# Kernel tuning notes

Measured on AMD Instinct MI355X. Metric: run time of the kernel, lower is better.

The kernel has to match this reference:

```python
import jax, jax.numpy as jnp
import numpy as np

EMBED_DIM = 1024
NUM_HEADS = 16
HEAD_DIM = EMBED_DIM // NUM_HEADS


def setup_inputs() -> dict:
    key = jax.random.key(0)
    ks = jax.random.split(key, 9)
    B, S, D = 4, 2048, EMBED_DIM
    scale = 1.0 / np.sqrt(D)
    inp = {
        "x": jax.random.normal(ks[0], (B, S, D), dtype=jnp.float32),
        "wq": jax.random.normal(ks[1], (D, D), dtype=jnp.float32) * scale,
        "bq": jnp.zeros((D,), dtype=jnp.float32),
        "wk": jax.random.normal(ks[2], (D, D), dtype=jnp.float32) * scale,
        "bk": jnp.zeros((D,), dtype=jnp.float32),
        "wv": jax.random.normal(ks[3], (D, D), dtype=jnp.float32) * scale,
        "bv": jnp.zeros((D,), dtype=jnp.float32),
        "wo": jax.random.normal(ks[4], (D, D), dtype=jnp.float32) * scale,
        "bo": jnp.zeros((D,), dtype=jnp.float32),
    }
    return inp


def reference(x, wq, bq, wk, bk, wv, bv, wo, bo):
    B, S, D = x.shape
    H, Hd = NUM_HEADS, HEAD_DIM

    def split_heads(t):
        # [B, S, D] -> [B, H, S, Hd]
        return t.reshape(B, S, H, Hd).transpose(0, 2, 1, 3)

    q = split_heads(x @ wq.T + bq)
    k = split_heads(x @ wk.T + bk)
    v = split_heads(x @ wv.T + bv)

    scores = jnp.einsum("bhqd,bhkd->bhqk", q, k) / jnp.sqrt(jnp.float32(Hd))
    attn = jax.nn.softmax(scores, axis=-1)
    out = jnp.einsum("bhqk,bhkd->bhqd", attn, v)  # [B, H, S, Hd]
    out = out.transpose(0, 2, 1, 3).reshape(B, S, D)
    return out @ wo.T + bo
```

## Files before the change

kernel.cpp:

```cpp
#include <hip/hip_runtime.h>
#include <hip/hip_bf16.h>
#include <hip/hip_fp16.h>

typedef _Float16 f16;
typedef f16 f16x8 __attribute__((ext_vector_type(8)));
typedef f16 f16x4 __attribute__((ext_vector_type(4)));
typedef f16 f16x2 __attribute__((ext_vector_type(2)));
typedef float f32x4 __attribute__((ext_vector_type(4)));
typedef float f32x16 __attribute__((ext_vector_type(16)));
typedef unsigned int u32x4 __attribute__((ext_vector_type(4)));
typedef unsigned int u32x2 __attribute__((ext_vector_type(2)));

#define MFMA16(a, b, c) __builtin_amdgcn_mfma_f32_16x16x32_f16(a, b, c, 0, 0, 0)
#define MFMA32(a, b, c) __builtin_amdgcn_mfma_f32_32x32x16_f16(a, b, c, 0, 0, 0)

constexpr int BB = 4, SS = 2048, DD = 1024, HH = 16, HDIM = 64;
constexpr int MM = BB * SS;
constexpr float QSCALE = 0.125f * 1.44269504088896340736f;


__device__ __forceinline__ void gl_lds16(const void* g, void* l) {
  __builtin_amdgcn_global_load_lds((const __attribute__((address_space(1))) void*)g,
                                   (__attribute__((address_space(3))) void*)l, 16, 0, 0);
}

__global__ __launch_bounds__(256) void cvt_all_kernel(const float* __restrict__ x,
                                                      const float* __restrict__ w0,
                                                      const float* __restrict__ w1,
                                                      const float* __restrict__ w2,
                                                      const float* __restrict__ w3,
                                                      f16* xh, f16* o0, f16* o1,
                                                      f16* o2, f16* o3) {
  int bid = blockIdx.x;
  const float* in; f16* out; int idx;
  if (bid < MM * DD / 4 / 256) {
    in = x; out = xh; idx = bid * 256 + threadIdx.x;
  } else {
    int wb = bid - MM * DD / 4 / 256;
    int which = wb >> 10;
    in = which == 0 ? w0 : which == 1 ? w1 : which == 2 ? w2 : w3;
    out = which == 0 ? o0 : which == 1 ? o1 : which == 2 ? o2 : o3;
    idx = (wb & 1023) * 256 + threadIdx.x;
  }
  f32x4 v = reinterpret_cast<const f32x4*>(in)[idx];
  f16x4 o;
  o[0] = (f16)v[0]; o[1] = (f16)v[1]; o[2] = (f16)v[2]; o[3] = (f16)v[3];
  reinterpret_cast<f16x4*>(out)[idx] = o;
}

__device__ __forceinline__ int swz(int row, int slot) {
  return row * 64 + ((slot ^ (row & 7)) << 3);
}

__global__ __launch_bounds__(256) void qkv_kernel(const f16* __restrict__ A,
                                                  const f16* __restrict__ Wq,
                                                  const f16* __restrict__ Wk,
                                                  const f16* __restrict__ Wv,
                                                  const float* __restrict__ bq,
                                                  const float* __restrict__ bk,
                                                  const float* __restrict__ bv,
                                                  f16* __restrict__ Qo,
                                                  f16* __restrict__ Ko,
                                                  f16* __restrict__ Vo) {
  constexpr int K = 1024;
  __shared__ __align__(16) char smem_raw[128 * 136 * 2];
  f16* As = (f16*)smem_raw;
  f16* Ws = As + 128 * 64;

  const int mat = blockIdx.x >> 3;
  const f16* W = mat == 0 ? Wq : (mat == 1 ? Wk : Wv);
  const float* bias = mat == 0 ? bq : (mat == 1 ? bk : bv);
  const float scale = mat == 0 ? QSCALE : 1.0f;

  const int tid = threadIdx.x;
  const int m0 = blockIdx.y * 128, n0 = (blockIdx.x & 7) * 128;
  const int w = tid >> 6, lane = tid & 63;
  const int wm = (w >> 1) * 64, wn = (w & 1) * 64;
  const int g = lane >> 4, r = lane & 15;
  const int srow = lane >> 3;
  const int sslot = (lane & 7) ^ srow;

  f32x4 acc[4][4] = {};

  for (int k0 = 0; k0 < K; k0 += 64) {
#pragma unroll
    for (int i = 0; i < 4; ++i) {
      int rbase = w * 32 + i * 8;
      gl_lds16(A + (size_t)(m0 + rbase + srow) * K + k0 + sslot * 8, As + rbase * 64);
      gl_lds16(W + (size_t)(n0 + rbase + srow) * K + k0 + sslot * 8, Ws + rbase * 64);
    }
    __syncthreads();

#pragma unroll
    for (int ks = 0; ks < 2; ++ks) {
      f16x8 af[4], bf[4];
#pragma unroll
      for (int i = 0; i < 4; ++i) {
        af[i] = *reinterpret_cast<const f16x8*>(As + swz(wm + i * 16 + r, (ks << 2) | g));
        bf[i] = *reinterpret_cast<const f16x8*>(Ws + swz(wn + i * 16 + r, (ks << 2) | g));
      }
#pragma unroll
      for (int i = 0; i < 4; ++i)
#pragma unroll
        for (int j = 0; j < 4; ++j)
          acc[i][j] = MFMA16(af[i], bf[j], acc[i][j]);
    }
    __syncthreads();
  }

  if (mat == 0) {
#pragma unroll
    for (int i = 0; i < 4; ++i)
#pragma unroll
      for (int j = 0; j < 4; ++j)
#pragma unroll
        for (int q = 0; q < 4; ++q) {
          int gm = m0 + wm + i * 16 + g * 4 + q;
          int gn = n0 + wn + j * 16 + r;
          float v = (acc[i][j][q] + bias[gn]) * scale;
          int b = gm >> 11, s = gm & 2047;
          int h = gn >> 6, hd = gn & 63;
          Qo[(((size_t)(b * HH + h)) * SS + s) * HDIM + hd] = (f16)v;
        }
  } else if (mat == 1) {
#pragma unroll
    for (int i = 0; i < 4; ++i)
#pragma unroll
      for (int j = 0; j < 4; ++j)
#pragma unroll
        for (int q = 0; q < 4; ++q) {
          int gm = m0 + wm + i * 16 + g * 4 + q;
          int gn = n0 + wn + j * 16 + r;
          float v = acc[i][j][q] + bias[gn];
          int b = gm >> 11, s = gm & 2047;
          int h = gn >> 6, hd = gn & 63;
          int tile = s >> 6, row = s & 63, slot = hd >> 3, w8 = hd & 7;
          size_t off = ((((size_t)(b * HH + h) * 32 + tile) * 8 + slot) * 64 + row) * 8 + w8;
          Ko[off] = (f16)v;
        }
  } else {
    __syncthreads();
    f16* T = (f16*)smem_raw;
#pragma unroll
    for (int i = 0; i < 4; ++i)
#pragma unroll
      for (int j = 0; j < 4; ++j)
#pragma unroll
        for (int q = 0; q < 4; ++q) {
          int ml = wm + i * 16 + g * 4 + q;
          int nl = wn + j * 16 + r;
          T[nl * 136 + ml] = (f16)(acc[i][j][q] + bias[n0 + nl]);
        }
    __syncthreads();
    const int b = m0 >> 11, sbase = m0 & 2047;
#pragma unroll
    for (int it = 0; it < 8; ++it) {
      int cid = it * 256 + tid;
      int hd_l = cid & 127, sl = (cid >> 7) & 7, tl = cid >> 10;
      u32x4 v = *reinterpret_cast<const u32x4*>(T + hd_l * 136 + tl * 64 + sl * 8);
      int gn = n0 + hd_l, h = gn >> 6, hd = gn & 63;
      int tile = (sbase >> 6) + tl;
      size_t off = ((((size_t)(b * HH + h) * 32 + tile) * 8 + sl) * 64 + hd) * 8;
      *reinterpret_cast<u32x4*>(Vo + off) = v;
    }
  }
}

__global__ __launch_bounds__(256) void oproj_kernel(const f16* __restrict__ A,
                                                    const f16* __restrict__ W,
                                                    const float* __restrict__ bias,
                                                    float* __restrict__ Out) {
  constexpr int K = 1024, N = 1024;
  __shared__ __align__(16) f16 As[128 * 64];
  __shared__ __align__(16) f16 Ws[128 * 64];

  const int tid = threadIdx.x;
  const int m0 = blockIdx.y * 128, n0 = blockIdx.x * 128;
  const int w = tid >> 6, lane = tid & 63;
  const int wm = (w >> 1) * 64, wn = (w & 1) * 64;
  const int g = lane >> 4, r = lane & 15;
  const int srow = lane >> 3;
  const int sslot = (lane & 7) ^ srow;

  f32x4 acc[4][4] = {};

  for (int k0 = 0; k0 < K; k0 += 64) {
#pragma unroll
    for (int i = 0; i < 4; ++i) {
      int rbase = w * 32 + i * 8;
      gl_lds16(A + (size_t)(m0 + rbase + srow) * K + k0 + sslot * 8, As + rbase * 64);
      gl_lds16(W + (size_t)(n0 + rbase + srow) * K + k0 + sslot * 8, Ws + rbase * 64);
    }
    __syncthreads();

#pragma unroll
    for (int ks = 0; ks < 2; ++ks) {
      f16x8 af[4], bf[4];
#pragma unroll
      for (int i = 0; i < 4; ++i) {
        af[i] = *reinterpret_cast<const f16x8*>(As + swz(wm + i * 16 + r, (ks << 2) | g));
        bf[i] = *reinterpret_cast<const f16x8*>(Ws + swz(wn + i * 16 + r, (ks << 2) | g));
      }
#pragma unroll
      for (int i = 0; i < 4; ++i)
#pragma unroll
        for (int j = 0; j < 4; ++j)
          acc[i][j] = MFMA16(af[i], bf[j], acc[i][j]);
    }
    __syncthreads();
  }

#pragma unroll
  for (int i = 0; i < 4; ++i)
#pragma unroll
    for (int j = 0; j < 4; ++j)
#pragma unroll
      for (int q = 0; q < 4; ++q) {
        int gm = m0 + wm + i * 16 + g * 4 + q;
        int gn = n0 + wn + j * 16 + r;
        Out[(size_t)gm * N + gn] = acc[i][j][q] + bias[gn];
      }
}

__global__ __launch_bounds__(256, 4) void attn_kernel(const f16* __restrict__ Q,
                                                      const f16* __restrict__ K,
                                                      const f16* __restrict__ Vt,
                                                      f16* __restrict__ AO) {
  __shared__ __align__(16) f16 Kls[2][8 * 512];
  __shared__ __align__(16) f16 Vls[2][8 * 512];
  __shared__ __align__(16) float Lw[4][32];

  const int tid = threadIdx.x;
  const int w = tid >> 6, lane = tid & 63;
  const int q31 = lane & 31;
  const int h = lane >> 5;
  const int bh = blockIdx.y;
  const int q0 = blockIdx.x * 128;

  const f16* Kg = K + (size_t)bh * (SS * HDIM);
  const f16* Vg = Vt + (size_t)bh * (SS * HDIM);
  const int s0 = 2 * w;
  const int rofs = h * 512 + q31 * 8;

  const f16* Qg = Q + ((size_t)bh * SS + q0 + w * 32 + q31) * HDIM + 8 * h;
  f16x8 qf[4];
#pragma unroll
  for (int m = 0; m < 4; ++m)
    qf[m] = *reinterpret_cast<const f16x8*>(Qg + 16 * m);

  f32x16 oacc[2] = {};
  float lsum = 0.f;

#pragma unroll
  for (int i = 0; i < 2; ++i) {
    int s_idx = s0 + i;
    gl_lds16(Kg + (size_t)(s_idx * 64 + lane) * 8, &Kls[0][s_idx * 512]);
    gl_lds16(Vg + (size_t)(s_idx * 64 + lane) * 8, &Vls[0][s_idx * 512]);
  }
  __syncthreads();

  for (int t = 0; t < SS / 64; ++t) {
    const int cur = t & 1;
    if (t < SS / 64 - 1) {
#pragma unroll
      for (int i = 0; i < 2; ++i) {
        int s_idx = s0 + i;
        gl_lds16(Kg + (size_t)((t + 1) * 512 + s_idx * 64 + lane) * 8,
                 &Kls[cur ^ 1][s_idx * 512]);
        gl_lds16(Vg + (size_t)((t + 1) * 512 + s_idx * 64 + lane) * 8,
                 &Vls[cur ^ 1][s_idx * 512]);
      }
    }
    const f16* Kc = &Kls[cur][0];
    const f16* Vc = &Vls[cur][0];

#pragma unroll
    for (int kb = 0; kb < 2; ++kb) {
      f32x16 sacc = {};
      __builtin_amdgcn_s_setprio(1);
#pragma unroll
      for (int m = 0; m < 4; ++m) {
        f16x8 kf = *reinterpret_cast<const f16x8*>(Kc + m * 1024 + kb * 256 + rofs);
        sacc = MFMA32(kf, qf[m], sacc);
      }
      __builtin_amdgcn_s_setprio(0);

      unsigned pk[8];
#pragma unroll
      for (int rp = 0; rp < 4; ++rp)
#pragma unroll
        for (int p = 0; p < 2; ++p) {
          float e0 = __builtin_amdgcn_exp2f(sacc[4 * rp + 2 * p]);
          float e1 = __builtin_amdgcn_exp2f(sacc[4 * rp + 2 * p + 1]);
          pk[2 * rp + p] = __builtin_bit_cast(unsigned, __builtin_amdgcn_cvt_pkrtz(e0, e1));
        }

      f16x2 s01 = __builtin_bit_cast(f16x2, pk[0]) + __builtin_bit_cast(f16x2, pk[1]);
      f16x2 s23 = __builtin_bit_cast(f16x2, pk[2]) + __builtin_bit_cast(f16x2, pk[3]);
      f16x2 s45 = __builtin_bit_cast(f16x2, pk[4]) + __builtin_bit_cast(f16x2, pk[5]);
      f16x2 s67 = __builtin_bit_cast(f16x2, pk[6]) + __builtin_bit_cast(f16x2, pk[7]);
      f16x2 st = (s01 + s23) + (s45 + s67);
      lsum += (float)st[0] + (float)st[1];

#pragma unroll
      for (int jl = 0; jl < 2; ++jl) {
        auto sw0 = __builtin_amdgcn_permlane32_swap(pk[4 * jl + 0], pk[4 * jl + 2], false, false);
        auto sw1 = __builtin_amdgcn_permlane32_swap(pk[4 * jl + 1], pk[4 * jl + 3], false, false);
        u32x4 fw = {(unsigned)sw0[0], (unsigned)sw1[0], (unsigned)sw0[1], (unsigned)sw1[1]};
        f16x8 pa = __builtin_bit_cast(f16x8, fw);
        const int j = 2 * kb + jl;
        __builtin_amdgcn_s_setprio(1);
#pragma unroll
        for (int vb = 0; vb < 2; ++vb) {
          f16x8 vbf = *reinterpret_cast<const f16x8*>(Vc + j * 1024 + vb * 256 + rofs);
          oacc[vb] = MFMA32(pa, vbf, oacc[vb]);
        }
        __builtin_amdgcn_s_setprio(0);
      }
    }
    __syncthreads();
  }

  lsum += __shfl_xor(lsum, 32, 64);
  if (h == 0) Lw[w][q31] = 1.0f / lsum;

  f32x4 li[4];
#pragma unroll
  for (int rq = 0; rq < 4; ++rq)
    li[rq] = *reinterpret_cast<const f32x4*>(&Lw[w][8 * rq + 4 * h]);

  const int b = bh >> 4, head = bh & 15;
  f16* aobase = AO + ((size_t)(b * SS + q0 + 32 * w)) * DD + head * 64 + q31;
#pragma unroll
  for (int vb = 0; vb < 2; ++vb)
#pragma unroll
    for (int reg = 0; reg < 16; ++reg) {
      int q = (reg & 3) + 8 * (reg >> 2) + 4 * h;
      aobase[(size_t)q * DD + 32 * vb] = (f16)(oacc[vb][reg] * li[reg >> 2][reg & 3]);
    }
}

extern "C" void kernel_launch(void* const* d_in, const int* in_sizes, int n_in,
                              void* d_out, int out_size, void* d_ws, size_t ws_size,
                              hipStream_t stream) {
  (void)in_sizes; (void)n_in; (void)out_size; (void)ws_size;
  const float* x  = (const float*)d_in[0];
  const float* wq = (const float*)d_in[1];
  const float* bq = (const float*)d_in[2];
  const float* wk = (const float*)d_in[3];
  const float* bk = (const float*)d_in[4];
  const float* wv = (const float*)d_in[5];
  const float* bv = (const float*)d_in[6];
  const float* wo = (const float*)d_in[7];
  const float* bo = (const float*)d_in[8];
  float* out = (float*)d_out;

  char* ws = (char*)d_ws;
  f16* xh  = (f16*)ws; ws += (size_t)MM * DD * 2;
  f16* wqh = (f16*)ws; ws += (size_t)DD * DD * 2;
  f16* wkh = (f16*)ws; ws += (size_t)DD * DD * 2;
  f16* wvh = (f16*)ws; ws += (size_t)DD * DD * 2;
  f16* woh = (f16*)ws; ws += (size_t)DD * DD * 2;
  f16* Qb  = (f16*)ws; ws += (size_t)MM * DD * 2;
  f16* Kb  = (f16*)ws; ws += (size_t)MM * DD * 2;
  f16* Vtb = (f16*)ws; ws += (size_t)MM * DD * 2;
  f16* AOb = (f16*)ws; ws += (size_t)MM * DD * 2;

  cvt_all_kernel<<<MM * DD / 4 / 256 + 4 * (DD * DD / 4 / 256), 256, 0, stream>>>(
      x, wq, wk, wv, wo, xh, wqh, wkh, wvh, woh);

  qkv_kernel<<<dim3(24, MM / 128), 256, 0, stream>>>(xh, wqh, wkh, wvh, bq, bk, bv, Qb, Kb, Vtb);

  attn_kernel<<<dim3(SS / 128, BB * HH), 256, 0, stream>>>(Qb, Kb, Vtb, AOb);

  oproj_kernel<<<dim3(DD / 128, MM / 128), 256, 0, stream>>>(AOb, woh, bo, out);
}
```

Baseline: 197.1 us.

## Stream K/V from global into registers, remap block order, coalesce K stores

The attention kernel drops its LDS double buffer and barriers and loads K and V fragments straight from global into registers, prefetching the next 32-key tile while the current one computes. All three GEMM and attention kernels switch to 1D grids with a remapped block order, so that consecutive blocks share the same rows or heads for better L2 locality. The K projection epilogue now goes through an LDS transpose and writes 16-byte vectors instead of scalars, and the LDS tile pitch grows to 152. Per-wave global loads give up the data sharing that LDS provided across the four waves, and they rely on the cache to absorb the repeated traffic.

```diff
diff --git a/kernel.cpp b/kernel.cpp
--- a/kernel.cpp
+++ b/kernel.cpp
@@ -63,17 +63,22 @@
                                                   f16* __restrict__ Ko,
                                                   f16* __restrict__ Vo) {
   constexpr int K = 1024;
-  __shared__ __align__(16) char smem_raw[128 * 136 * 2];
+  constexpr int TS = 152;
+  __shared__ __align__(16) char smem_raw[128 * TS * 2];
   f16* As = (f16*)smem_raw;
   f16* Ws = As + 128 * 64;
 
-  const int mat = blockIdx.x >> 3;
+  const int p = blockIdx.x;
+  const int bx = (p >> 3) % 24;
+  const int by = (p & 7) + 8 * ((p >> 3) / 24);
+
+  const int mat = bx >> 3;
   const f16* W = mat == 0 ? Wq : (mat == 1 ? Wk : Wv);
   const float* bias = mat == 0 ? bq : (mat == 1 ? bk : bv);
   const float scale = mat == 0 ? QSCALE : 1.0f;
 
   const int tid = threadIdx.x;
-  const int m0 = blockIdx.y * 128, n0 = (blockIdx.x & 7) * 128;
+  const int m0 = by * 128, n0 = (bx & 7) * 128;
   const int w = tid >> 6, lane = tid & 63;
   const int wm = (w >> 1) * 64, wn = (w & 1) * 64;
   const int g = lane >> 4, r = lane & 15;
@@ -123,22 +128,6 @@
           Qo[(((size_t)(b * HH + h)) * SS + s) * HDIM + hd] = (f16)v;
         }
   } else if (mat == 1) {
-#pragma unroll
-    for (int i = 0; i < 4; ++i)
-#pragma unroll
-      for (int j = 0; j < 4; ++j)
-#pragma unroll
-        for (int q = 0; q < 4; ++q) {
-          int gm = m0 + wm + i * 16 + g * 4 + q;
-          int gn = n0 + wn + j * 16 + r;
-          float v = acc[i][j][q] + bias[gn];
-          int b = gm >> 11, s = gm & 2047;
-          int h = gn >> 6, hd = gn & 63;
-          int tile = s >> 6, row = s & 63, slot = hd >> 3, w8 = hd & 7;
-          size_t off = ((((size_t)(b * HH + h) * 32 + tile) * 8 + slot) * 64 + row) * 8 + w8;
-          Ko[off] = (f16)v;
-        }
-  } else {
     __syncthreads();
     f16* T = (f16*)smem_raw;
 #pragma unroll
@@ -149,7 +138,33 @@
         for (int q = 0; q < 4; ++q) {
           int ml = wm + i * 16 + g * 4 + q;
           int nl = wn + j * 16 + r;
-          T[nl * 136 + ml] = (f16)(acc[i][j][q] + bias[n0 + nl]);
+          T[ml * TS + nl] = (f16)(acc[i][j][q] + bias[n0 + nl]);
+        }
+    __syncthreads();
+    const int b = m0 >> 11, sbase = m0 & 2047;
+#pragma unroll
+    for (int it = 0; it < 8; ++it) {
+      int cid = it * 256 + tid;
+      int row_s = cid & 127, ns = cid >> 7;
+      u32x4 v = *reinterpret_cast<const u32x4*>(T + row_s * TS + ns * 8);
+      int gn0 = n0 + ns * 8;
+      int h = gn0 >> 6, slot = (gn0 & 63) >> 3;
+      int tile = (sbase >> 6) + (row_s >> 6), row = row_s & 63;
+      size_t off = ((((size_t)(b * HH + h) * 32 + tile) * 8 + slot) * 64 + row) * 8;
+      *reinterpret_cast<u32x4*>(Ko + off) = v;
+    }
+  } else {
+    __syncthreads();
+    f16* T = (f16*)smem_raw;
+#pragma unroll
+    for (int i = 0; i < 4; ++i)
+#pragma unroll
+      for (int j = 0; j < 4; ++j)
+#pragma unroll
+        for (int q = 0; q < 4; ++q) {
+          int ml = wm + i * 16 + g * 4 + q;
+          int nl = wn + j * 16 + r;
+          T[nl * TS + ml] = (f16)(acc[i][j][q] + bias[n0 + nl]);
         }
     __syncthreads();
     const int b = m0 >> 11, sbase = m0 & 2047;
@@ -157,7 +172,7 @@
     for (int it = 0; it < 8; ++it) {
       int cid = it * 256 + tid;
       int hd_l = cid & 127, sl = (cid >> 7) & 7, tl = cid >> 10;
-      u32x4 v = *reinterpret_cast<const u32x4*>(T + hd_l * 136 + tl * 64 + sl * 8);
+      u32x4 v = *reinterpret_cast<const u32x4*>(T + hd_l * TS + tl * 64 + sl * 8);
       int gn = n0 + hd_l, h = gn >> 6, hd = gn & 63;
       int tile = (sbase >> 6) + tl;
       size_t off = ((((size_t)(b * HH + h) * 32 + tile) * 8 + sl) * 64 + hd) * 8;
@@ -174,8 +189,12 @@
   __shared__ __align__(16) f16 As[128 * 64];
   __shared__ __align__(16) f16 Ws[128 * 64];
 
+  const int p = blockIdx.x;
+  const int bx = (p >> 3) & 7;
+  const int by = (p & 7) | ((p >> 6) << 3);
+
   const int tid = threadIdx.x;
-  const int m0 = blockIdx.y * 128, n0 = blockIdx.x * 128;
+  const int m0 = by * 128, n0 = bx * 128;
   const int w = tid >> 6, lane = tid & 63;
   const int wm = (w >> 1) * 64, wn = (w & 1) * 64;
   const int g = lane >> 4, r = lane & 15;
@@ -226,21 +245,20 @@
                                                       const f16* __restrict__ K,
                                                       const f16* __restrict__ Vt,
                                                       f16* __restrict__ AO) {
-  __shared__ __align__(16) f16 Kls[2][8 * 512];
-  __shared__ __align__(16) f16 Vls[2][8 * 512];
-  __shared__ __align__(16) float Lw[4][32];
+  __shared__ float Lw[4][32];
+
+  const int p = blockIdx.x;
+  const int qx = (p >> 3) & 15;
+  const int bh = (p & 7) | ((p >> 7) << 3);
+  const int q0 = qx * 128;
 
   const int tid = threadIdx.x;
   const int w = tid >> 6, lane = tid & 63;
   const int q31 = lane & 31;
   const int h = lane >> 5;
-  const int bh = blockIdx.y;
-  const int q0 = blockIdx.x * 128;
-
-  const f16* Kg = K + (size_t)bh * (SS * HDIM);
-  const f16* Vg = Vt + (size_t)bh * (SS * HDIM);
-  const int s0 = 2 * w;
-  const int rofs = h * 512 + q31 * 8;
+
+  const f16* Kl = K + (size_t)bh * (SS * HDIM) + h * 512 + q31 * 8;
+  const f16* Vl = Vt + (size_t)bh * (SS * HDIM) + h * 512 + q31 * 8;
 
   const f16* Qg = Q + ((size_t)bh * SS + q0 + w * 32 + q31) * HDIM + 8 * h;
   f16x8 qf[4];
@@ -250,75 +268,72 @@
 
   f32x16 oacc[2] = {};
   float lsum = 0.f;
-
-#pragma unroll
-  for (int i = 0; i < 2; ++i) {
-    int s_idx = s0 + i;
-    gl_lds16(Kg + (size_t)(s_idx * 64 + lane) * 8, &Kls[0][s_idx * 512]);
-    gl_lds16(Vg + (size_t)(s_idx * 64 + lane) * 8, &Vls[0][s_idx * 512]);
-  }
-  __syncthreads();
-
-  for (int t = 0; t < SS / 64; ++t) {
-    const int cur = t & 1;
-    if (t < SS / 64 - 1) {
-#pragma unroll
-      for (int i = 0; i < 2; ++i) {
-        int s_idx = s0 + i;
-        gl_lds16(Kg + (size_t)((t + 1) * 512 + s_idx * 64 + lane) * 8,
-                 &Kls[cur ^ 1][s_idx * 512]);
-        gl_lds16(Vg + (size_t)((t + 1) * 512 + s_idx * 64 + lane) * 8,
-                 &Vls[cur ^ 1][s_idx * 512]);
+  unsigned pk[8];
+
+  u32x4 kc[4], vc[4];
+
+#define LD16(PTR) (*reinterpret_cast<const u32x4*>(PTR))
+#define KOFF(T) ((size_t)((T) >> 1) * 4096 + ((T)&1) * 256)
+
+#pragma unroll
+  for (int m = 0; m < 4; ++m) kc[m] = LD16(Kl + m * 1024);
+#pragma unroll
+  for (int j = 0; j < 2; ++j)
+#pragma unroll
+    for (int vb = 0; vb < 2; ++vb) vc[2 * j + vb] = LD16(Vl + j * 1024 + vb * 256);
+
+  for (int t = 0; t < SS / 32; ++t) {
+    f32x16 sacc = {};
+    __builtin_amdgcn_s_setprio(1);
+#pragma unroll
+    for (int m = 0; m < 4; ++m)
+      sacc = MFMA32(__builtin_bit_cast(f16x8, kc[m]), qf[m], sacc);
+    __builtin_amdgcn_s_setprio(0);
+
+    if (t < SS / 32 - 1) {
+      const size_t ko = KOFF(t + 1);
+#pragma unroll
+      for (int m = 0; m < 4; ++m) kc[m] = LD16(Kl + ko + m * 1024);
+    }
+
+#pragma unroll
+    for (int rp = 0; rp < 4; ++rp)
+#pragma unroll
+      for (int pp = 0; pp < 2; ++pp) {
+        float e0 = __builtin_amdgcn_exp2f(sacc[4 * rp + 2 * pp]);
+        float e1 = __builtin_amdgcn_exp2f(sacc[4 * rp + 2 * pp + 1]);
+        pk[2 * rp + pp] = __builtin_bit_cast(unsigned, __builtin_amdgcn_cvt_pkrtz(e0, e1));
       }
-    }
-    const f16* Kc = &Kls[cur][0];
-    const f16* Vc = &Vls[cur][0];
-
-#pragma unroll
-    for (int kb = 0; kb < 2; ++kb) {
-      f32x16 sacc = {};
-      __builtin_amdgcn_s_setprio(1);
-#pragma unroll
-      for (int m = 0; m < 4; ++m) {
-        f16x8 kf = *reinterpret_cast<const f16x8*>(Kc + m * 1024 + kb * 256 + rofs);
-        sacc = MFMA32(kf, qf[m], sacc);
-      }
-      __builtin_amdgcn_s_setprio(0);
-
-      unsigned pk[8];
-#pragma unroll
-      for (int rp = 0; rp < 4; ++rp)
-#pragma unroll
-        for (int p = 0; p < 2; ++p) {
-          float e0 = __builtin_amdgcn_exp2f(sacc[4 * rp + 2 * p]);
-          float e1 = __builtin_amdgcn_exp2f(sacc[4 * rp + 2 * p + 1]);
-          pk[2 * rp + p] = __builtin_bit_cast(unsigned, __builtin_amdgcn_cvt_pkrtz(e0, e1));
-        }
-
-      f16x2 s01 = __builtin_bit_cast(f16x2, pk[0]) + __builtin_bit_cast(f16x2, pk[1]);
-      f16x2 s23 = __builtin_bit_cast(f16x2, pk[2]) + __builtin_bit_cast(f16x2, pk[3]);
-      f16x2 s45 = __builtin_bit_cast(f16x2, pk[4]) + __builtin_bit_cast(f16x2, pk[5]);
-      f16x2 s67 = __builtin_bit_cast(f16x2, pk[6]) + __builtin_bit_cast(f16x2, pk[7]);
-      f16x2 st = (s01 + s23) + (s45 + s67);
-      lsum += (float)st[0] + (float)st[1];
-
-#pragma unroll
-      for (int jl = 0; jl < 2; ++jl) {
-        auto sw0 = __builtin_amdgcn_permlane32_swap(pk[4 * jl + 0], pk[4 * jl + 2], false, false);
-        auto sw1 = __builtin_amdgcn_permlane32_swap(pk[4 * jl + 1], pk[4 * jl + 3], false, false);
-        u32x4 fw = {(unsigned)sw0[0], (unsigned)sw1[0], (unsigned)sw0[1], (unsigned)sw1[1]};
-        f16x8 pa = __builtin_bit_cast(f16x8, fw);
-        const int j = 2 * kb + jl;
-        __builtin_amdgcn_s_setprio(1);
-#pragma unroll
-        for (int vb = 0; vb < 2; ++vb) {
-          f16x8 vbf = *reinterpret_cast<const f16x8*>(Vc + j * 1024 + vb * 256 + rofs);
-          oacc[vb] = MFMA32(pa, vbf, oacc[vb]);
-        }
-        __builtin_amdgcn_s_setprio(0);
-      }
-    }
-    __syncthreads();
+    {
+      f16x2 u01 = __builtin_bit_cast(f16x2, pk[0]) + __builtin_bit_cast(f16x2, pk[1]);
+      f16x2 u23 = __builtin_bit_cast(f16x2, pk[2]) + __builtin_bit_cast(f16x2, pk[3]);
+      f16x2 u45 = __builtin_bit_cast(f16x2, pk[4]) + __builtin_bit_cast(f16x2, pk[5]);
+      f16x2 u67 = __builtin_bit_cast(f16x2, pk[6]) + __builtin_bit_cast(f16x2, pk[7]);
+      f16x2 ut = (u01 + u23) + (u45 + u67);
+      lsum += (float)ut[0] + (float)ut[1];
+    }
+
+    __builtin_amdgcn_s_setprio(1);
+#pragma unroll
+    for (int j = 0; j < 2; ++j) {
+      auto s0 = __builtin_amdgcn_permlane32_swap(pk[4 * j + 0], pk[4 * j + 2], false, false);
+      auto s1 = __builtin_amdgcn_permlane32_swap(pk[4 * j + 1], pk[4 * j + 3], false, false);
+      u32x4 fw = {(unsigned)s0[0], (unsigned)s1[0], (unsigned)s0[1], (unsigned)s1[1]};
+      f16x8 pa = __builtin_bit_cast(f16x8, fw);
+#pragma unroll
+      for (int vb = 0; vb < 2; ++vb)
+        oacc[vb] = MFMA32(pa, __builtin_bit_cast(f16x8, vc[2 * j + vb]), oacc[vb]);
+    }
+    __builtin_amdgcn_s_setprio(0);
+
+    if (t < SS / 32 - 1) {
+      const size_t vo = (size_t)(t + 1) * 2048;
+#pragma unroll
+      for (int j = 0; j < 2; ++j)
+#pragma unroll
+        for (int vb = 0; vb < 2; ++vb)
+          vc[2 * j + vb] = LD16(Vl + vo + j * 1024 + vb * 256);
+    }
   }
 
   lsum += __shfl_xor(lsum, 32, 64);
@@ -338,6 +353,8 @@
       int q = (reg & 3) + 8 * (reg >> 2) + 4 * h;
       aobase[(size_t)q * DD + 32 * vb] = (f16)(oacc[vb][reg] * li[reg >> 2][reg & 3]);
     }
+#undef LD16
+#undef KOFF
 }
 
 extern "C" void kernel_launch(void* const* d_in, const int* in_sizes, int n_in,
@@ -369,9 +386,9 @@
   cvt_all_kernel<<<MM * DD / 4 / 256 + 4 * (DD * DD / 4 / 256), 256, 0, stream>>>(
       x, wq, wk, wv, wo, xh, wqh, wkh, wvh, woh);
 
-  qkv_kernel<<<dim3(24, MM / 128), 256, 0, stream>>>(xh, wqh, wkh, wvh, bq, bk, bv, Qb, Kb, Vtb);
-
-  attn_kernel<<<dim3(SS / 128, BB * HH), 256, 0, stream>>>(Qb, Kb, Vtb, AOb);
-
-  oproj_kernel<<<dim3(DD / 128, MM / 128), 256, 0, stream>>>(AOb, woh, bo, out);
-}
+  qkv_kernel<<<1536, 256, 0, stream>>>(xh, wqh, wkh, wvh, bq, bk, bv, Qb, Kb, Vtb);
+
+  attn_kernel<<<1024, 256, 0, stream>>>(Qb, Kb, Vtb, AOb);
+
+  oproj_kernel<<<512, 256, 0, stream>>>(AOb, woh, bo, out);
+}
```

New measurement: 199.3 us. No clear change (+1.2%).
